# Optimization experiments

Hardware: AMD Instinct MI355X
Metric: run time of the kernel (lower is better)

The kernel has to match this reference:

```python
import jax, jax.numpy as jnp
import numpy as np

HIDDEN_DIM = 64
TIER_SPECS = [(4, 64), (8, 32), (16, 16)]
VOCAB_SIZE = 64
B = 131072


def setup_inputs() -> dict:
    key = jax.random.key(0)
    ks = jax.random.split(key, 16)
    inp = {
        "query_h": jax.random.normal(ks[0], (B, HIDDEN_DIM), dtype=jnp.float32),
        "mem0": jax.random.normal(ks[1], (B, 4, 64), dtype=jnp.float32),
        "mem1": jax.random.normal(ks[2], (B, 8, 32), dtype=jnp.float32),
        "mem2": jax.random.normal(ks[3], (B, 16, 16), dtype=jnp.float32),
    }
    # per-tier down-proj (HIDDEN->dim) and up-proj (dim->HIDDEN), torch Linear layout [out,in]
    for i, (_, dim) in enumerate(TIER_SPECS):
        s = 1.0 / np.sqrt(HIDDEN_DIM)
        inp[f"Wp{i}"] = jax.random.uniform(ks[4 + i], (dim, HIDDEN_DIM), minval=-s, maxval=s, dtype=jnp.float32)
        inp[f"bp{i}"] = jax.random.uniform(ks[7 + i], (dim,), minval=-s, maxval=s, dtype=jnp.float32)
        su = 1.0 / np.sqrt(dim)
        inp[f"Wu{i}"] = jax.random.uniform(ks[10 + i], (HIDDEN_DIM, dim), minval=-su, maxval=su, dtype=jnp.float32)
        inp[f"bu{i}"] = jax.random.uniform(ks[13 + i], (HIDDEN_DIM,), minval=-su, maxval=su, dtype=jnp.float32)
    sc = 1.0 / np.sqrt(HIDDEN_DIM)
    inp["Wc"] = jax.random.uniform(jax.random.fold_in(key, 99), (VOCAB_SIZE, HIDDEN_DIM), minval=-sc, maxval=sc, dtype=jnp.float32)
    inp["bc"] = jax.random.uniform(jax.random.fold_in(key, 100), (VOCAB_SIZE,), minval=-sc, maxval=sc, dtype=jnp.float32)
    return inp


def _tier(q, mem, Wp, bp, Wu, bu, dim):
    qp = q @ Wp.T + bp                                   # [B, dim]
    sims = jnp.einsum('bsd,bd->bs', mem, qp) / (dim ** 0.5)  # [B, S]
    w = jax.nn.softmax(sims, axis=-1)
    conf = w.max(axis=-1)                                # [B]
    retrieved = jnp.einsum('bs,bsd->bd', w, mem)         # [B, dim]
    return retrieved @ Wu.T + bu, conf                   # [B, HIDDEN], [B]


def reference(query_h, mem0, mem1, mem2,
              Wp0, bp0, Wp1, bp1, Wp2, bp2,
              Wu0, bu0, Wu1, bu1, Wu2, bu2, Wc, bc):
    mems = [mem0, mem1, mem2]
    Wps, bps = [Wp0, Wp1, Wp2], [bp0, bp1, bp2]
    Wus, bus = [Wu0, Wu1, Wu2], [bu0, bu1, bu2]
    results, confs = [], []
    for i, (_, dim) in enumerate(TIER_SPECS):
        r, c = _tier(query_h, mems[i], Wps[i], bps[i], Wus[i], bus[i], dim)
        results.append(r)
        confs.append(c)
    confs = jax.nn.softmax(jnp.stack(confs, axis=1), axis=-1)  # [B, 3]
    result = sum(confs[:, i:i + 1] * results[i] for i in range(3))
    return result @ Wc.T + bc
```

## Files before the change

### kernel.cpp

```cpp
#include <hip/hip_runtime.h>

#define NROWS 131072
#define GRID1 1024
#define ITERS 8

__device__ __forceinline__ float dot4(float4 a, float4 b) {
    return fmaf(a.x, b.x, fmaf(a.y, b.y, fmaf(a.z, b.z, a.w * b.w)));
}

struct Smem {
    float Wp[112 * 68];
    float bpb[112];
    float Waug[64 * 116];
    float qbuf[4][4][64];
    float qpbuf[4][4][112];
    float rbuf[4][4][116];
};

template<int SEG>
__device__ __forceinline__ float tier_proc(int lane, float4 m, const float* qpbase, float* rbase) {
    float4 qpv = *reinterpret_cast<const float4*>(qpbase + 4 * (lane & (SEG - 1)));
    float p = dot4(m, qpv);
#pragma unroll
    for (int off = 1; off < SEG; off <<= 1) p += __shfl_xor(p, off, 64);
    float mx = p;
#pragma unroll
    for (int off = SEG; off < 64; off <<= 1) mx = fmaxf(mx, __shfl_xor(mx, off, 64));
    float e = __expf(p - mx);
    float den = e;
#pragma unroll
    for (int off = SEG; off < 64; off <<= 1) den += __shfl_xor(den, off, 64);
    float4 rv = make_float4(m.x * e, m.y * e, m.z * e, m.w * e);
#pragma unroll
    for (int off = SEG; off < 64; off <<= 1) {
        rv.x += __shfl_xor(rv.x, off, 64);
        rv.y += __shfl_xor(rv.y, off, 64);
        rv.z += __shfl_xor(rv.z, off, 64);
        rv.w += __shfl_xor(rv.w, off, 64);
    }
    if (lane < SEG) *reinterpret_cast<float4*>(rbase + 4 * lane) = rv;
    return den;
}

__global__ __launch_bounds__(128) void prep_kernel(
    const float* __restrict__ Wu0, const float* __restrict__ Wu1, const float* __restrict__ Wu2,
    const float* __restrict__ bu0, const float* __restrict__ bu1, const float* __restrict__ bu2,
    const float* __restrict__ Wc,  const float* __restrict__ bc,  float* __restrict__ waug) {
    int o = blockIdx.x;
    int c = threadIdx.x;
    if (c >= 116) return;
    float acc = 0.0f;
    if (c < 112) {
        const float* wu; int d, dim;
        if (c < 64)      { wu = Wu0; d = c;      dim = 64; }
        else if (c < 96) { wu = Wu1; d = c - 64; dim = 32; }
        else             { wu = Wu2; d = c - 96; dim = 16; }
        for (int h = 0; h < 64; ++h) acc = fmaf(Wc[o * 64 + h], wu[h * dim + d], acc);
    } else if (c < 115) {
        const float* bu = (c == 112) ? bu0 : (c == 113) ? bu1 : bu2;
        for (int h = 0; h < 64; ++h) acc = fmaf(Wc[o * 64 + h], bu[h], acc);
    } else {
        acc = bc[o];
    }
    waug[o * 116 + c] = acc;
}

__global__ __launch_bounds__(256, 2) void retrieval_kernel(
    const float* __restrict__ query,
    const float* __restrict__ mem0, const float* __restrict__ mem1, const float* __restrict__ mem2,
    const float* __restrict__ Wp0, const float* __restrict__ bp0,
    const float* __restrict__ Wp1, const float* __restrict__ bp1,
    const float* __restrict__ Wp2, const float* __restrict__ bp2,
    const float* __restrict__ waug, float* __restrict__ out) {
    __shared__ Smem sm;
    const int t = threadIdx.x;
    const int wv = t >> 6;
    const int lane = t & 63;

    for (int idx = t; idx < 4096; idx += 256) { int r = idx >> 6, k = idx & 63; sm.Wp[r * 68 + k] = Wp0[idx] * 0.125f; }
    for (int idx = t; idx < 2048; idx += 256) { int r = idx >> 6, k = idx & 63; sm.Wp[(64 + r) * 68 + k] = Wp1[idx] * 0.17677669529663687f; }
    for (int idx = t; idx < 1024; idx += 256) { int r = idx >> 6, k = idx & 63; sm.Wp[(96 + r) * 68 + k] = Wp2[idx] * 0.25f; }
    if (t < 112) {
        float sc = (t < 64) ? 0.125f : (t < 96) ? 0.17677669529663687f : 0.25f;
        float v  = (t < 64) ? bp0[t] : (t < 96) ? bp1[t - 64] : bp2[t - 96];
        sm.bpb[t] = v * sc;
    }
    for (int idx = t; idx < 7424; idx += 256) sm.Waug[idx] = waug[idx];
    __syncthreads();

    const float4* w0p = reinterpret_cast<const float4*>(&sm.Wp[lane * 68]);
    const float4* w1p = reinterpret_cast<const float4*>(&sm.Wp[(64 + (lane & 31)) * 68]);
    const float4* w2p = reinterpret_cast<const float4*>(&sm.Wp[(96 + (lane & 15)) * 68]);
    const float4* war = reinterpret_cast<const float4*>(&sm.Waug[lane * 116]);
    const float b0 = sm.bpb[lane];
    const float b1 = sm.bpb[64 + (lane & 31)];
    const float b2 = sm.bpb[96 + (lane & 15)];

    const int blockRow0 = blockIdx.x * (ITERS * 16);

    for (int it = 0; it < ITERS; ++it) {
        const int r0 = blockRow0 + it * 16 + wv * 4;

        float4 mpre[3][4];
#pragma unroll
        for (int j = 0; j < 4; ++j) {
            sm.qbuf[wv][j][lane] = query[(r0 + j) * 64 + lane];
        }
#pragma unroll
        for (int j = 0; j < 4; ++j) {
            mpre[0][j] = reinterpret_cast<const float4*>(mem0 + (size_t)(r0 + j) * 256)[lane];
            mpre[1][j] = reinterpret_cast<const float4*>(mem1 + (size_t)(r0 + j) * 256)[lane];
            mpre[2][j] = reinterpret_cast<const float4*>(mem2 + (size_t)(r0 + j) * 256)[lane];
        }

        float a0[4], a1[4], a2[4];
#pragma unroll
        for (int j = 0; j < 4; ++j) { a0[j] = b0; a1[j] = b1; a2[j] = b2; }
#pragma unroll 4
        for (int kb = 0; kb < 16; ++kb) {
            float4 w0 = w0p[kb], w1 = w1p[kb], w2 = w2p[kb];
#pragma unroll
            for (int j = 0; j < 4; ++j) {
                float4 qv = reinterpret_cast<const float4*>(&sm.qbuf[wv][j][0])[kb];
                a0[j] = fmaf(w0.x, qv.x, fmaf(w0.y, qv.y, fmaf(w0.z, qv.z, fmaf(w0.w, qv.w, a0[j]))));
                a1[j] = fmaf(w1.x, qv.x, fmaf(w1.y, qv.y, fmaf(w1.z, qv.z, fmaf(w1.w, qv.w, a1[j]))));
                a2[j] = fmaf(w2.x, qv.x, fmaf(w2.y, qv.y, fmaf(w2.z, qv.z, fmaf(w2.w, qv.w, a2[j]))));
            }
        }
#pragma unroll
        for (int j = 0; j < 4; ++j) {
            sm.qpbuf[wv][j][lane] = a0[j];
            if (lane < 32) sm.qpbuf[wv][j][64 + lane] = a1[j];
            if (lane < 16) sm.qpbuf[wv][j][96 + lane] = a2[j];
        }

        float cf0[4], cf1[4], cf2[4];
#pragma unroll
        for (int j = 0; j < 4; ++j) {
            float* qp = &sm.qpbuf[wv][j][0];
            float* rb = &sm.rbuf[wv][j][0];
            float den0 = tier_proc<16>(lane, mpre[0][j], qp, rb);
            float den1 = tier_proc<8>(lane, mpre[1][j], qp + 64, rb + 64);
            float den2 = tier_proc<4>(lane, mpre[2][j], qp + 96, rb + 96);
            float c0 = __frcp_rn(den0), c1 = __frcp_rn(den1), c2 = __frcp_rn(den2);
            float cm = fmaxf(c0, fmaxf(c1, c2));
            float e0 = __expf(c0 - cm), e1 = __expf(c1 - cm), e2 = __expf(c2 - cm);
            float ics = __frcp_rn(e0 + e1 + e2);
            float cw0 = e0 * ics, cw1 = e1 * ics, cw2 = e2 * ics;
            cf0[j] = cw0 * c0;
            cf1[j] = cw1 * c1;
            cf2[j] = cw2 * c2;
            float ext = (lane == 0) ? cw0 : (lane == 1) ? cw1 : (lane == 2) ? cw2 : 1.0f;
            if (lane < 4) rb[112 + lane] = ext;
        }

        float t0[4] = {0, 0, 0, 0}, t1[4] = {0, 0, 0, 0}, t2[4] = {0, 0, 0, 0}, t3[4];
#pragma unroll 4
        for (int cb = 0; cb < 16; ++cb) {
            float4 w = war[cb];
#pragma unroll
            for (int j = 0; j < 4; ++j) {
                float4 rv = reinterpret_cast<const float4*>(&sm.rbuf[wv][j][0])[cb];
                t0[j] = fmaf(w.x, rv.x, fmaf(w.y, rv.y, fmaf(w.z, rv.z, fmaf(w.w, rv.w, t0[j]))));
            }
        }
#pragma unroll 4
        for (int cb = 16; cb < 24; ++cb) {
            float4 w = war[cb];
#pragma unroll
            for (int j = 0; j < 4; ++j) {
                float4 rv = reinterpret_cast<const float4*>(&sm.rbuf[wv][j][0])[cb];
                t1[j] = fmaf(w.x, rv.x, fmaf(w.y, rv.y, fmaf(w.z, rv.z, fmaf(w.w, rv.w, t1[j]))));
            }
        }
#pragma unroll
        for (int cb = 24; cb < 28; ++cb) {
            float4 w = war[cb];
#pragma unroll
            for (int j = 0; j < 4; ++j) {
                float4 rv = reinterpret_cast<const float4*>(&sm.rbuf[wv][j][0])[cb];
                t2[j] = fmaf(w.x, rv.x, fmaf(w.y, rv.y, fmaf(w.z, rv.z, fmaf(w.w, rv.w, t2[j]))));
            }
        }
        {
            float4 w = war[28];
#pragma unroll
            for (int j = 0; j < 4; ++j) {
                float4 rv = reinterpret_cast<const float4*>(&sm.rbuf[wv][j][0])[28];
                t3[j] = dot4(w, rv);
            }
        }
#pragma unroll
        for (int j = 0; j < 4; ++j) {
            out[(r0 + j) * 64 + lane] =
                fmaf(cf0[j], t0[j], fmaf(cf1[j], t1[j], fmaf(cf2[j], t2[j], t3[j])));
        }
    }
}

extern "C" void kernel_launch(void* const* d_in, const int* in_sizes, int n_in,
                              void* d_out, int out_size, void* d_ws, size_t ws_size,
                              hipStream_t stream) {
    const float* query = (const float*)d_in[0];
    const float* mem0  = (const float*)d_in[1];
    const float* mem1  = (const float*)d_in[2];
    const float* mem2  = (const float*)d_in[3];
    const float* Wp0   = (const float*)d_in[4];
    const float* bp0   = (const float*)d_in[5];
    const float* Wu0   = (const float*)d_in[6];
    const float* bu0   = (const float*)d_in[7];
    const float* Wp1   = (const float*)d_in[8];
    const float* bp1   = (const float*)d_in[9];
    const float* Wu1   = (const float*)d_in[10];
    const float* bu1   = (const float*)d_in[11];
    const float* Wp2   = (const float*)d_in[12];
    const float* bp2   = (const float*)d_in[13];
    const float* Wu2   = (const float*)d_in[14];
    const float* bu2   = (const float*)d_in[15];
    const float* Wc    = (const float*)d_in[16];
    const float* bc    = (const float*)d_in[17];
    float* waug = (float*)d_ws;
    float* outp = (float*)d_out;

    prep_kernel<<<64, 128, 0, stream>>>(Wu0, Wu1, Wu2, bu0, bu1, bu2, Wc, bc, waug);
    retrieval_kernel<<<GRID1, 256, 0, stream>>>(query, mem0, mem1, mem2,
                                                Wp0, bp0, Wp1, bp1, Wp2, bp2,
                                                waug, outp);
}
```

Baseline: 552.8 us.

## Remap memory lanes to use DPP row ops and read query directly from global

Memory rows are loaded with a permuted lane-to-element mapping so that the softmax max, denominator and weighted-sum reductions over slots run on lanes inside a DPP row. That lets them use DPP row instructions (quad xor, half-mirror, row rotate) instead of cross-lane shuffles that go through LDS. The dot-product sums across each slot now use ROR DPP plus two shuffles. The query staging buffer in shared memory is also removed, and the projection reads query float4s directly from global memory, trusting the cache to serve the broadcast loads. The permuted loads may reduce coalescing, and the uniform global query loads add memory latency to the inner loop.

```diff
diff --git a/kernel.cpp b/kernel.cpp
--- a/kernel.cpp
+++ b/kernel.cpp
@@ -3,6 +3,19 @@
 #define NROWS 131072
 #define GRID1 1024
 #define ITERS 8
+
+#define DPP_XOR1 0xB1
+#define DPP_XOR2 0x4E
+#define DPP_HMIR 0x141
+#define DPP_ROR1 0x121
+#define DPP_ROR2 0x122
+#define DPP_ROR4 0x124
+#define DPP_ROR8 0x128
+
+template<int C>
+__device__ __forceinline__ float fdpp(float x) {
+    return __int_as_float(__builtin_amdgcn_mov_dpp(__float_as_int(x), C, 0xF, 0xF, true));
+}
 
 __device__ __forceinline__ float dot4(float4 a, float4 b) {
     return fmaf(a.x, b.x, fmaf(a.y, b.y, fmaf(a.z, b.z, a.w * b.w)));
@@ -12,33 +25,79 @@
     float Wp[112 * 68];
     float bpb[112];
     float Waug[64 * 116];
-    float qbuf[4][4][64];
     float qpbuf[4][4][112];
     float rbuf[4][4][116];
 };
 
-template<int SEG>
-__device__ __forceinline__ float tier_proc(int lane, float4 m, const float* qpbase, float* rbase) {
-    float4 qpv = *reinterpret_cast<const float4*>(qpbase + 4 * (lane & (SEG - 1)));
-    float p = dot4(m, qpv);
-#pragma unroll
-    for (int off = 1; off < SEG; off <<= 1) p += __shfl_xor(p, off, 64);
-    float mx = p;
-#pragma unroll
-    for (int off = SEG; off < 64; off <<= 1) mx = fmaxf(mx, __shfl_xor(mx, off, 64));
+__device__ __forceinline__ float tier0_proc(int lane, float4 m, const float* qp, float* rb) {
+    float4 qv = *reinterpret_cast<const float4*>(qp + 4 * (lane >> 2));
+    float p = dot4(m, qv);
+    p += fdpp<DPP_ROR4>(p);
+    p += fdpp<DPP_ROR8>(p);
+    p += __shfl_xor(p, 16, 64);
+    p += __shfl_xor(p, 32, 64);
+    float mx = fmaxf(p, fdpp<DPP_XOR1>(p));
+    mx = fmaxf(mx, fdpp<DPP_XOR2>(mx));
     float e = __expf(p - mx);
-    float den = e;
-#pragma unroll
-    for (int off = SEG; off < 64; off <<= 1) den += __shfl_xor(den, off, 64);
+    float den = e + fdpp<DPP_XOR1>(e);
+    den += fdpp<DPP_XOR2>(den);
     float4 rv = make_float4(m.x * e, m.y * e, m.z * e, m.w * e);
-#pragma unroll
-    for (int off = SEG; off < 64; off <<= 1) {
-        rv.x += __shfl_xor(rv.x, off, 64);
-        rv.y += __shfl_xor(rv.y, off, 64);
-        rv.z += __shfl_xor(rv.z, off, 64);
-        rv.w += __shfl_xor(rv.w, off, 64);
-    }
-    if (lane < SEG) *reinterpret_cast<float4*>(rbase + 4 * lane) = rv;
+    rv.x += fdpp<DPP_XOR1>(rv.x); rv.y += fdpp<DPP_XOR1>(rv.y);
+    rv.z += fdpp<DPP_XOR1>(rv.z); rv.w += fdpp<DPP_XOR1>(rv.w);
+    rv.x += fdpp<DPP_XOR2>(rv.x); rv.y += fdpp<DPP_XOR2>(rv.y);
+    rv.z += fdpp<DPP_XOR2>(rv.z); rv.w += fdpp<DPP_XOR2>(rv.w);
+    if ((lane & 3) == 0) *reinterpret_cast<float4*>(rb + 4 * (lane >> 2)) = rv;
+    return den;
+}
+
+__device__ __forceinline__ float tier1_proc(int lane, float4 m, const float* qp, float* rb) {
+    float4 qv = *reinterpret_cast<const float4*>(qp + 4 * (lane >> 3));
+    float p = dot4(m, qv);
+    p += fdpp<DPP_ROR8>(p);
+    p += __shfl_xor(p, 16, 64);
+    p += __shfl_xor(p, 32, 64);
+    float mx = fmaxf(p, fdpp<DPP_XOR1>(p));
+    mx = fmaxf(mx, fdpp<DPP_XOR2>(mx));
+    mx = fmaxf(mx, fdpp<DPP_HMIR>(mx));
+    float e = __expf(p - mx);
+    float den = e + fdpp<DPP_XOR1>(e);
+    den += fdpp<DPP_XOR2>(den);
+    den += fdpp<DPP_HMIR>(den);
+    float4 rv = make_float4(m.x * e, m.y * e, m.z * e, m.w * e);
+    rv.x += fdpp<DPP_XOR1>(rv.x); rv.y += fdpp<DPP_XOR1>(rv.y);
+    rv.z += fdpp<DPP_XOR1>(rv.z); rv.w += fdpp<DPP_XOR1>(rv.w);
+    rv.x += fdpp<DPP_XOR2>(rv.x); rv.y += fdpp<DPP_XOR2>(rv.y);
+    rv.z += fdpp<DPP_XOR2>(rv.z); rv.w += fdpp<DPP_XOR2>(rv.w);
+    rv.x += fdpp<DPP_HMIR>(rv.x); rv.y += fdpp<DPP_HMIR>(rv.y);
+    rv.z += fdpp<DPP_HMIR>(rv.z); rv.w += fdpp<DPP_HMIR>(rv.w);
+    if ((lane & 7) == 0) *reinterpret_cast<float4*>(rb + 4 * (lane >> 3)) = rv;
+    return den;
+}
+
+__device__ __forceinline__ float tier2_proc(int lane, float4 m, const float* qp, float* rb) {
+    float4 qv = *reinterpret_cast<const float4*>(qp + 4 * (lane >> 4));
+    float p = dot4(m, qv);
+    p += __shfl_xor(p, 16, 64);
+    p += __shfl_xor(p, 32, 64);
+    float mx = fmaxf(p, fdpp<DPP_ROR1>(p));
+    mx = fmaxf(mx, fdpp<DPP_ROR2>(mx));
+    mx = fmaxf(mx, fdpp<DPP_ROR4>(mx));
+    mx = fmaxf(mx, fdpp<DPP_ROR8>(mx));
+    float e = __expf(p - mx);
+    float den = e + fdpp<DPP_ROR1>(e);
+    den += fdpp<DPP_ROR2>(den);
+    den += fdpp<DPP_ROR4>(den);
+    den += fdpp<DPP_ROR8>(den);
+    float4 rv = make_float4(m.x * e, m.y * e, m.z * e, m.w * e);
+    rv.x += fdpp<DPP_ROR1>(rv.x); rv.y += fdpp<DPP_ROR1>(rv.y);
+    rv.z += fdpp<DPP_ROR1>(rv.z); rv.w += fdpp<DPP_ROR1>(rv.w);
+    rv.x += fdpp<DPP_ROR2>(rv.x); rv.y += fdpp<DPP_ROR2>(rv.y);
+    rv.z += fdpp<DPP_ROR2>(rv.z); rv.w += fdpp<DPP_ROR2>(rv.w);
+    rv.x += fdpp<DPP_ROR4>(rv.x); rv.y += fdpp<DPP_ROR4>(rv.y);
+    rv.z += fdpp<DPP_ROR4>(rv.z); rv.w += fdpp<DPP_ROR4>(rv.w);
+    rv.x += fdpp<DPP_ROR8>(rv.x); rv.y += fdpp<DPP_ROR8>(rv.y);
+    rv.z += fdpp<DPP_ROR8>(rv.z); rv.w += fdpp<DPP_ROR8>(rv.w);
+    if ((lane & 15) == 0) *reinterpret_cast<float4*>(rb + 4 * (lane >> 4)) = rv;
     return den;
 }
 
@@ -96,6 +155,10 @@
     const float b1 = sm.bpb[64 + (lane & 31)];
     const float b2 = sm.bpb[96 + (lane & 15)];
 
+    const int mi0 = 16 * (lane & 3)  + (lane >> 2);
+    const int mi1 = 8  * (lane & 7)  + (lane >> 3);
+    const int mi2 = 4  * (lane & 15) + (lane >> 4);
+
     const int blockRow0 = blockIdx.x * (ITERS * 16);
 
     for (int it = 0; it < ITERS; ++it) {
@@ -104,28 +167,34 @@
         float4 mpre[3][4];
 #pragma unroll
         for (int j = 0; j < 4; ++j) {
-            sm.qbuf[wv][j][lane] = query[(r0 + j) * 64 + lane];
-        }
-#pragma unroll
-        for (int j = 0; j < 4; ++j) {
-            mpre[0][j] = reinterpret_cast<const float4*>(mem0 + (size_t)(r0 + j) * 256)[lane];
-            mpre[1][j] = reinterpret_cast<const float4*>(mem1 + (size_t)(r0 + j) * 256)[lane];
-            mpre[2][j] = reinterpret_cast<const float4*>(mem2 + (size_t)(r0 + j) * 256)[lane];
-        }
-
+            mpre[0][j] = reinterpret_cast<const float4*>(mem0 + (size_t)(r0 + j) * 256)[mi0];
+            mpre[1][j] = reinterpret_cast<const float4*>(mem1 + (size_t)(r0 + j) * 256)[mi1];
+            mpre[2][j] = reinterpret_cast<const float4*>(mem2 + (size_t)(r0 + j) * 256)[mi2];
+        }
+
+        const float4* qg0 = reinterpret_cast<const float4*>(query + (size_t)(r0 + 0) * 64);
+        const float4* qg1 = reinterpret_cast<const float4*>(query + (size_t)(r0 + 1) * 64);
+        const float4* qg2 = reinterpret_cast<const float4*>(query + (size_t)(r0 + 2) * 64);
+        const float4* qg3 = reinterpret_cast<const float4*>(query + (size_t)(r0 + 3) * 64);
         float a0[4], a1[4], a2[4];
 #pragma unroll
         for (int j = 0; j < 4; ++j) { a0[j] = b0; a1[j] = b1; a2[j] = b2; }
 #pragma unroll 4
         for (int kb = 0; kb < 16; ++kb) {
             float4 w0 = w0p[kb], w1 = w1p[kb], w2 = w2p[kb];
-#pragma unroll
-            for (int j = 0; j < 4; ++j) {
-                float4 qv = reinterpret_cast<const float4*>(&sm.qbuf[wv][j][0])[kb];
-                a0[j] = fmaf(w0.x, qv.x, fmaf(w0.y, qv.y, fmaf(w0.z, qv.z, fmaf(w0.w, qv.w, a0[j]))));
-                a1[j] = fmaf(w1.x, qv.x, fmaf(w1.y, qv.y, fmaf(w1.z, qv.z, fmaf(w1.w, qv.w, a1[j]))));
-                a2[j] = fmaf(w2.x, qv.x, fmaf(w2.y, qv.y, fmaf(w2.z, qv.z, fmaf(w2.w, qv.w, a2[j]))));
-            }
+            float4 qv0 = qg0[kb], qv1 = qg1[kb], qv2 = qg2[kb], qv3 = qg3[kb];
+            a0[0] = fmaf(w0.x, qv0.x, fmaf(w0.y, qv0.y, fmaf(w0.z, qv0.z, fmaf(w0.w, qv0.w, a0[0]))));
+            a1[0] = fmaf(w1.x, qv0.x, fmaf(w1.y, qv0.y, fmaf(w1.z, qv0.z, fmaf(w1.w, qv0.w, a1[0]))));
+            a2[0] = fmaf(w2.x, qv0.x, fmaf(w2.y, qv0.y, fmaf(w2.z, qv0.z, fmaf(w2.w, qv0.w, a2[0]))));
+            a0[1] = fmaf(w0.x, qv1.x, fmaf(w0.y, qv1.y, fmaf(w0.z, qv1.z, fmaf(w0.w, qv1.w, a0[1]))));
+            a1[1] = fmaf(w1.x, qv1.x, fmaf(w1.y, qv1.y, fmaf(w1.z, qv1.z, fmaf(w1.w, qv1.w, a1[1]))));
+            a2[1] = fmaf(w2.x, qv1.x, fmaf(w2.y, qv1.y, fmaf(w2.z, qv1.z, fmaf(w2.w, qv1.w, a2[1]))));
+            a0[2] = fmaf(w0.x, qv2.x, fmaf(w0.y, qv2.y, fmaf(w0.z, qv2.z, fmaf(w0.w, qv2.w, a0[2]))));
+            a1[2] = fmaf(w1.x, qv2.x, fmaf(w1.y, qv2.y, fmaf(w1.z, qv2.z, fmaf(w1.w, qv2.w, a1[2]))));
+            a2[2] = fmaf(w2.x, qv2.x, fmaf(w2.y, qv2.y, fmaf(w2.z, qv2.z, fmaf(w2.w, qv2.w, a2[2]))));
+            a0[3] = fmaf(w0.x, qv3.x, fmaf(w0.y, qv3.y, fmaf(w0.z, qv3.z, fmaf(w0.w, qv3.w, a0[3]))));
+            a1[3] = fmaf(w1.x, qv3.x, fmaf(w1.y, qv3.y, fmaf(w1.z, qv3.z, fmaf(w1.w, qv3.w, a1[3]))));
+            a2[3] = fmaf(w2.x, qv3.x, fmaf(w2.y, qv3.y, fmaf(w2.z, qv3.z, fmaf(w2.w, qv3.w, a2[3]))));
         }
 #pragma unroll
         for (int j = 0; j < 4; ++j) {
@@ -139,9 +208,9 @@
         for (int j = 0; j < 4; ++j) {
             float* qp = &sm.qpbuf[wv][j][0];
             float* rb = &sm.rbuf[wv][j][0];
-            float den0 = tier_proc<16>(lane, mpre[0][j], qp, rb);
-            float den1 = tier_proc<8>(lane, mpre[1][j], qp + 64, rb + 64);
-            float den2 = tier_proc<4>(lane, mpre[2][j], qp + 96, rb + 96);
+            float den0 = tier0_proc(lane, mpre[0][j], qp, rb);
+            float den1 = tier1_proc(lane, mpre[1][j], qp + 64, rb + 64);
+            float den2 = tier2_proc(lane, mpre[2][j], qp + 96, rb + 96);
             float c0 = __frcp_rn(den0), c1 = __frcp_rn(den1), c2 = __frcp_rn(den2);
             float cm = fmaxf(c0, fmaxf(c1, c2));
             float e0 = __expf(c0 - cm), e1 = __expf(c1 - cm), e2 = __expf(c2 - cm);
```

Result: faster. 536.8 us (-2.9%).
